# Kernel tuning notes

Measured on AMD Instinct MI355X. Metric: run time of the kernel, lower is better.

The kernel has to match this reference:

```python
import jax, jax.numpy as jnp
import numpy as np

B, N, M, D, OUT, K = 8, 32, 64, 128, 128, 3
EPS = 1e-5


def batchnorm(x, g, b):
    # training-mode BatchNorm2d over NCHW (stats over B,H,W per channel, biased var)
    mean = x.mean((0, 2, 3), keepdims=True)
    var = ((x - mean) ** 2).mean((0, 2, 3), keepdims=True)
    return g[None, :, None, None] * (x - mean) * jax.lax.rsqrt(var + EPS) + b[None, :, None, None]


def mycorr(x):
    # Pearson correlation between nodes along feature dim: x (B,M,N,D) -> (B,M,N,N)
    xc = x - x.mean(-1, keepdims=True)
    num = jnp.einsum('bmid,bmjd->bmij', xc, xc)
    nrm = jnp.sqrt((xc * xc).sum(-1))
    return num / (nrm[:, :, :, None] * nrm[:, :, None, :] + 1e-8)


def attention(x, W_fc1, W_fc2):
    # x: (B,M,N,D). AdaptiveAvgPool2d((None,1)) over the concat [Wh_i, pos*Wh_j]
    # equals 0.5*(mean_d Wh_i + mean_d(pos*Wh_j)); pos=1 where Wh_i==Wh_j else 2.
    adj = mycorr(x)
    mean_i = x.mean(-1)                       # (B,M,N)
    xi = x[:, :, :, None, :]                  # (B,M,N,1,D)
    xj = x[:, :, None, :, :]                  # (B,M,1,N,D)
    alt_mean = jnp.where(xi == xj, xj, 2.0 * xj).mean(-1)  # (B,M,N,N)
    e = 0.5 * (mean_i[:, :, :, None] + alt_mean)            # (B,M,N,N)
    ef = e.reshape(e.shape[0], e.shape[1], -1)              # (B,M,N*N) pair channels
    h = jax.nn.relu(jnp.einsum('rp,bmp->bmr', W_fc1, ef))
    e2 = jax.nn.sigmoid(jnp.einsum('pr,bmr->bmp', W_fc2, h)).reshape(e.shape)
    att = jax.nn.softmax(jnp.where(adj > 0, e2, jnp.float32(-1e12)), axis=-1)
    return jnp.einsum('bmij,bmjd->bmid', att, x)


def setup_inputs() -> dict:
    key = jax.random.key(0)
    ks = jax.random.split(key, 8)
    P, r, s = N * N, (N * N) // 2, 0.05
    return {
        'x': jax.random.normal(ks[0], (B, N, M, D), jnp.float32),
        'W_sc': jax.random.normal(ks[1], (OUT, M), jnp.float32) * s,
        'g_sc': jnp.ones(OUT, jnp.float32), 'b_sc': jnp.zeros(OUT, jnp.float32),
        'W_l1': jax.random.normal(ks[2], (M, M), jnp.float32) * s,
        'g1': jnp.ones(M, jnp.float32), 'b1': jnp.zeros(M, jnp.float32),
        'W_fc1': jax.random.normal(ks[3], (r, P), jnp.float32) * s,
        'W_fc2': jax.random.normal(ks[4], (P, r), jnp.float32) * s,
        'g2': jnp.ones(M, jnp.float32), 'b2': jnp.zeros(M, jnp.float32),
        'W_dw': jax.random.normal(ks[5], (N, 1, K, K), jnp.float32) * s,
        'g3': jnp.ones(N, jnp.float32), 'b3': jnp.zeros(N, jnp.float32),
        'W_l3': jax.random.normal(ks[6], (OUT, M), jnp.float32) * s,
    }


def reference(x, W_sc, g_sc, b_sc, W_l1, g1, b1, W_fc1, W_fc2, g2, b2, W_dw, g3, b3, W_l3):
    xm = jnp.transpose(x, (0, 2, 1, 3))  # (B,M,N,D)
    # shortcut: 1x1 conv over head channel + BN (stride=1 path)
    shortcut = batchnorm(jnp.einsum('om,bmnd->bond', W_sc, xm), g_sc, b_sc)
    # layer_1: 1x1 conv, BN, global node attention, BN, ReLU
    out = batchnorm(jnp.einsum('cm,bmnd->bcnd', W_l1, xm), g1, b1)
    out = attention(out, W_fc1, W_fc2)
    out = jax.nn.relu(batchnorm(out, g2, b2))
    # layer_2: depthwise KxK conv over (head, dim) per node, BN, ReLU
    out = jnp.transpose(out, (0, 2, 1, 3))  # (B,N,M,D)
    pad = K // 2
    out = jax.lax.conv_general_dilated(out, W_dw, (1, 1), ((pad, pad), (pad, pad)),
                                       feature_group_count=N,
                                       dimension_numbers=('NCHW', 'OIHW', 'NCHW'))
    out = jax.nn.relu(batchnorm(out, g3, b3))
    # layer_3: 1x1 conv to out_channels heads + residual
    out = jnp.transpose(out, (0, 2, 1, 3))  # (B,M,N,D)
    out = jnp.einsum('om,bmnd->bond', W_l3, out) + shortcut
    return jnp.transpose(out, (0, 2, 1, 3))  # (B,N,OUT,D)
```

## Files before the change

kernel.cpp:

```cpp
#include <hip/hip_runtime.h>
#include <math.h>

#define EPS 1e-5f


__device__ __forceinline__ void fma4(float4& a, float s, const float4& v) {
    a.x += s * v.x; a.y += s * v.y; a.z += s * v.z; a.w += s * v.w;
}

__global__ __launch_bounds__(256) void k1_w(
    const float* __restrict__ x, const float* __restrict__ Wsc,
    const float* __restrict__ Wl1, float* __restrict__ t_sc,
    float* __restrict__ t_l1, float* __restrict__ stats)
{
    int g  = blockIdx.x;
    int bn = blockIdx.y;
    int b = bn >> 5, n = bn & 31;
    __shared__ __align__(16) float s_x[64 * 128];
    __shared__ __align__(16) float s_wT[64 * 68];
    int t = threadIdx.x;

    const float4* xg = (const float4*)(x + (size_t)bn * 8192);
    for (int i = t; i < 2048; i += 256) ((float4*)s_x)[i] = xg[i];

    const float* wbase = (g < 2) ? (Wsc + (size_t)g * 64 * 64) : Wl1;
    for (int i = t; i < 1024; i += 256) {
        int m = i >> 4, rq = (i & 15) * 4;
        float4 wv;
        wv.x = wbase[(size_t)(rq + 0) * 64 + m];
        wv.y = wbase[(size_t)(rq + 1) * 64 + m];
        wv.z = wbase[(size_t)(rq + 2) * 64 + m];
        wv.w = wbase[(size_t)(rq + 3) * 64 + m];
        *(float4*)(s_wT + m * 68 + rq) = wv;
    }
    __syncthreads();

    int wv = t >> 6, lane = t & 63;
    int dl = lane & 15, g4 = lane >> 4;
    int d0 = dl * 8;
    int c0 = wv * 16 + g4 * 4;

    float4 acc[4][2];
#pragma unroll
    for (int i = 0; i < 4; i++) { acc[i][0] = make_float4(0,0,0,0); acc[i][1] = make_float4(0,0,0,0); }

    for (int m = 0; m < 64; m += 2) {
        float4 x00 = *(const float4*)(s_x + m * 128 + d0);
        float4 x01 = *(const float4*)(s_x + m * 128 + d0 + 4);
        float4 x10 = *(const float4*)(s_x + (m + 1) * 128 + d0);
        float4 x11 = *(const float4*)(s_x + (m + 1) * 128 + d0 + 4);
        float4 w0 = *(const float4*)(s_wT + m * 68 + c0);
        float4 w1 = *(const float4*)(s_wT + (m + 1) * 68 + c0);
        fma4(acc[0][0], w0.x, x00); fma4(acc[0][1], w0.x, x01);
        fma4(acc[1][0], w0.y, x00); fma4(acc[1][1], w0.y, x01);
        fma4(acc[2][0], w0.z, x00); fma4(acc[2][1], w0.z, x01);
        fma4(acc[3][0], w0.w, x00); fma4(acc[3][1], w0.w, x01);
        fma4(acc[0][0], w1.x, x10); fma4(acc[0][1], w1.x, x11);
        fma4(acc[1][0], w1.y, x10); fma4(acc[1][1], w1.y, x11);
        fma4(acc[2][0], w1.z, x10); fma4(acc[2][1], w1.z, x11);
        fma4(acc[3][0], w1.w, x10); fma4(acc[3][1], w1.w, x11);
    }

#pragma unroll
    for (int i = 0; i < 4; i++) {
        int cc = g * 64 + c0 + i;
        float4 v0 = acc[i][0], v1 = acc[i][1];
        float* dst;
        if (cc < 128) dst = t_sc + (((size_t)(b * 128 + cc)) * 32 + n) * 128 + d0;
        else          dst = t_l1 + (((size_t)(b * 64 + (cc - 128))) * 32 + n) * 128 + d0;
        *(float4*)dst = v0;
        *(float4*)(dst + 4) = v1;
        float s = v0.x + v0.y + v0.z + v0.w + v1.x + v1.y + v1.z + v1.w;
        float q = v0.x*v0.x + v0.y*v0.y + v0.z*v0.z + v0.w*v0.w
                + v1.x*v1.x + v1.y*v1.y + v1.z*v1.z + v1.w*v1.w;
#pragma unroll
        for (int off = 8; off > 0; off >>= 1) {
            s += __shfl_down(s, off, 16);
            q += __shfl_down(q, off, 16);
        }
        if (dl == 0) {
            if (cc < 128) {
                atomicAdd(&stats[cc], s);
                atomicAdd(&stats[cc + 128], q);
            } else {
                atomicAdd(&stats[256 + (cc - 128)], s);
                atomicAdd(&stats[320 + (cc - 128)], q);
            }
        }
    }
}

__global__ __launch_bounds__(256) void k2_w(
    const float* __restrict__ t_l1, const float* __restrict__ g1,
    const float* __restrict__ b1, const float* __restrict__ stats,
    float* __restrict__ y_g, float* __restrict__ E,
    unsigned int* __restrict__ maskbits)
{
    int blk = blockIdx.x;
    int bm = blk >> 1, h = blk & 1;
    int t  = threadIdx.x;
    __shared__ __align__(16) float y_s[32 * 132];
    __shared__ float S_s[32];
    __shared__ unsigned int m_s[16];
    int m = bm & 63;
    float mean = stats[256 + m] * (1.0f / 32768.0f);
    float var  = stats[320 + m] * (1.0f / 32768.0f) - mean * mean;
    float a = g1[m] * rsqrtf(var + EPS);
    float c = b1[m] - a * mean;

    if (t < 16) m_s[t] = 0u;
    const float4* src = (const float4*)(t_l1 + (size_t)bm * 4096);
    for (int i = t; i < 1024; i += 256) {
        float4 v = src[i];
        v.x = a * v.x + c; v.y = a * v.y + c; v.z = a * v.z + c; v.w = a * v.w + c;
        *(float4*)(y_s + (i >> 5) * 132 + (i & 31) * 4) = v;
    }
    __syncthreads();

    {
        int r = t >> 3, j = t & 7;
        float s = 0.f;
        const float* yr = y_s + r * 132 + j * 16;
#pragma unroll
        for (int dd = 0; dd < 16; dd++) s += yr[dd];
#pragma unroll
        for (int off = 4; off > 0; off >>= 1) s += __shfl_down(s, off, 8);
        if (j == 0) S_s[r] = s;
    }
    __syncthreads();

    int i_loc = t >> 4;
    int i = h * 16 + i_loc;
    int j0 = (t & 15) * 2;
    float dot0 = 0.f, dot1 = 0.f, eq0 = 0.f, eq1 = 0.f;
    const float* yi  = y_s + i * 132;
    const float* yj0 = y_s + j0 * 132;
    const float* yj1 = y_s + (j0 + 1) * 132;
    for (int dq = 0; dq < 32; dq++) {
        float4 a4 = *(const float4*)(yi + dq * 4);
        float4 b0 = *(const float4*)(yj0 + dq * 4);
        float4 b1v = *(const float4*)(yj1 + dq * 4);
        dot0 += a4.x * b0.x + a4.y * b0.y + a4.z * b0.z + a4.w * b0.w;
        eq0  += (a4.x == b0.x ? b0.x : 0.f) + (a4.y == b0.y ? b0.y : 0.f)
              + (a4.z == b0.z ? b0.z : 0.f) + (a4.w == b0.w ? b0.w : 0.f);
        dot1 += a4.x * b1v.x + a4.y * b1v.y + a4.z * b1v.z + a4.w * b1v.w;
        eq1  += (a4.x == b1v.x ? b1v.x : 0.f) + (a4.y == b1v.y ? b1v.y : 0.f)
              + (a4.z == b1v.z ? b1v.z : 0.f) + (a4.w == b1v.w ? b1v.w : 0.f);
    }
    float Si = S_s[i];
    float Sj0 = S_s[j0], Sj1 = S_s[j0 + 1];
    unsigned int bits = 0u;
    if (dot0 - Si * Sj0 * (1.0f / 128.0f) > 0.f) bits |= (1u << j0);
    if (dot1 - Si * Sj1 * (1.0f / 128.0f) > 0.f) bits |= (1u << (j0 + 1));
    float ev0 = (Si + 2.f * Sj0 - eq0) * (1.0f / 256.0f);
    float ev1 = (Si + 2.f * Sj1 - eq1) * (1.0f / 256.0f);
    atomicOr(&m_s[i_loc], bits);
    *(float2*)(E + (size_t)bm * 1024 + i * 32 + j0) = make_float2(ev0, ev1);
    __syncthreads();
    if (t < 16) maskbits[bm * 32 + h * 16 + t] = m_s[t];

    float4* yd = (float4*)(y_g + (size_t)bm * 4096);
    for (int idx = t; idx < 512; idx += 256) {
        int row = h * 16 + (idx >> 5), col = (idx & 31) * 4;
        yd[h * 512 + idx] = *(const float4*)(y_s + row * 132 + col);
    }
}

__global__ __launch_bounds__(256) void k3a_w(
    const float* __restrict__ A, const float* __restrict__ Bm,
    float* __restrict__ Cp)
{
    __shared__ __align__(16) float lds[4 * 2304];
    int blk = blockIdx.x;
    int kz = blk >> 8, tile = blk & 255;
    int ct = tile & 15, rt = tile >> 4;
    const float* Ab = A + kz * 512;
    const float* Bb = Bm + kz * 512;
    float* C = Cp + (size_t)kz * 262144;
    int t = threadIdx.x;
    int w = t >> 6, l = t & 63;
    int row0 = rt * 32, col0 = ct * 32;
    float* As = lds + w * 2304;
    float* Bs = As + 1152;
    int rg = l >> 3, cg = l & 7, kq = (l & 7) * 4;
    const int SLABS = 4, KROW = 1024;

    float4 acc[4];
#pragma unroll
    for (int ii = 0; ii < 4; ii++) acc[ii] = make_float4(0,0,0,0);

    float4 av[4], bv[4], av2[4], bv2[4];
    int k0 = w * 32;
#pragma unroll
    for (int rr = 0; rr < 4; rr++) {
        int r = rg + rr * 8;
        av[rr] = *(const float4*)(Ab + (size_t)(row0 + r) * KROW + k0 + kq);
        bv[rr] = *(const float4*)(Bb + (size_t)(col0 + r) * KROW + k0 + kq);
    }
    for (int s = 0; s < SLABS; s++) {
#pragma unroll
        for (int rr = 0; rr < 4; rr++) {
            int r = rg + rr * 8;
            As[(kq + 0) * 36 + r] = av[rr].x; As[(kq + 1) * 36 + r] = av[rr].y;
            As[(kq + 2) * 36 + r] = av[rr].z; As[(kq + 3) * 36 + r] = av[rr].w;
            Bs[(kq + 0) * 36 + r] = bv[rr].x; Bs[(kq + 1) * 36 + r] = bv[rr].y;
            Bs[(kq + 2) * 36 + r] = bv[rr].z; Bs[(kq + 3) * 36 + r] = bv[rr].w;
        }
        if (s + 1 < SLABS) {
            int kn = (4 * (s + 1) + w) * 32;
#pragma unroll
            for (int rr = 0; rr < 4; rr++) {
                int r = rg + rr * 8;
                av2[rr] = *(const float4*)(Ab + (size_t)(row0 + r) * KROW + kn + kq);
                bv2[rr] = *(const float4*)(Bb + (size_t)(col0 + r) * KROW + kn + kq);
            }
        }
#pragma unroll
        for (int k = 0; k < 32; k++) {
            float4 a = *(const float4*)(As + k * 36 + rg * 4);
            float4 b = *(const float4*)(Bs + k * 36 + cg * 4);
            fma4(acc[0], a.x, b); fma4(acc[1], a.y, b);
            fma4(acc[2], a.z, b); fma4(acc[3], a.w, b);
        }
#pragma unroll
        for (int rr = 0; rr < 4; rr++) { av[rr] = av2[rr]; bv[rr] = bv2[rr]; }
    }

    __syncthreads();
    float* red = lds;
#pragma unroll
    for (int ii = 0; ii < 4; ii++)
        *(float4*)(red + w * 1024 + (rg * 4 + ii) * 32 + cg * 4) = acc[ii];
    __syncthreads();

    int r = t >> 3, c4 = (t & 7) * 4;
    float4 s0 = *(const float4*)(red + r * 32 + c4);
    float4 s1 = *(const float4*)(red + 1024 + r * 32 + c4);
    float4 s2 = *(const float4*)(red + 2048 + r * 32 + c4);
    float4 s3 = *(const float4*)(red + 3072 + r * 32 + c4);
    float4 v;
    v.x = s0.x + s1.x + s2.x + s3.x;
    v.y = s0.y + s1.y + s2.y + s3.y;
    v.z = s0.z + s1.z + s2.z + s3.z;
    v.w = s0.w + s1.w + s2.w + s3.w;
    *(float4*)(C + (size_t)(row0 + r) * 512 + col0 + c4) = v;
}

__global__ __launch_bounds__(256) void k4a_w(
    const float* __restrict__ H0, const float* __restrict__ H1,
    const float* __restrict__ Bm, float* __restrict__ Cp)
{
    __shared__ __align__(16) float lds[4 * 2304];
    int blk = blockIdx.x;
    int kz = blk >> 9, tile = blk & 511;
    int ct = tile & 31, rt = tile >> 5;
    const float* H0b = H0 + kz * 256;
    const float* H1b = H1 + kz * 256;
    const float* Bb  = Bm + kz * 256;
    float* C = Cp + (size_t)kz * 524288;
    int t = threadIdx.x;
    int w = t >> 6, l = t & 63;
    int row0 = rt * 32, col0 = ct * 32;
    float* As = lds + w * 2304;
    float* Bs = As + 1152;
    int rg = l >> 3, cg = l & 7, kq = (l & 7) * 4;
    const int SLABS = 2, KROW = 512;

    float4 acc[4];
#pragma unroll
    for (int ii = 0; ii < 4; ii++) acc[ii] = make_float4(0,0,0,0);

    float4 av[4], bv[4], av2[4], bv2[4];
    int k0 = w * 32;
#pragma unroll
    for (int rr = 0; rr < 4; rr++) {
        int r = rg + rr * 8;
        size_t ai = (size_t)(row0 + r) * KROW + k0 + kq;
        float4 h0 = *(const float4*)(H0b + ai);
        float4 h1 = *(const float4*)(H1b + ai);
        av[rr].x = fmaxf(h0.x + h1.x, 0.f); av[rr].y = fmaxf(h0.y + h1.y, 0.f);
        av[rr].z = fmaxf(h0.z + h1.z, 0.f); av[rr].w = fmaxf(h0.w + h1.w, 0.f);
        bv[rr] = *(const float4*)(Bb + (size_t)(col0 + r) * KROW + k0 + kq);
    }
    for (int s = 0; s < SLABS; s++) {
#pragma unroll
        for (int rr = 0; rr < 4; rr++) {
            int r = rg + rr * 8;
            As[(kq + 0) * 36 + r] = av[rr].x; As[(kq + 1) * 36 + r] = av[rr].y;
            As[(kq + 2) * 36 + r] = av[rr].z; As[(kq + 3) * 36 + r] = av[rr].w;
            Bs[(kq + 0) * 36 + r] = bv[rr].x; Bs[(kq + 1) * 36 + r] = bv[rr].y;
            Bs[(kq + 2) * 36 + r] = bv[rr].z; Bs[(kq + 3) * 36 + r] = bv[rr].w;
        }
        if (s + 1 < SLABS) {
            int kn = (4 * (s + 1) + w) * 32;
#pragma unroll
            for (int rr = 0; rr < 4; rr++) {
                int r = rg + rr * 8;
                size_t ai = (size_t)(row0 + r) * KROW + kn + kq;
                float4 h0 = *(const float4*)(H0b + ai);
                float4 h1 = *(const float4*)(H1b + ai);
                av2[rr].x = fmaxf(h0.x + h1.x, 0.f); av2[rr].y = fmaxf(h0.y + h1.y, 0.f);
                av2[rr].z = fmaxf(h0.z + h1.z, 0.f); av2[rr].w = fmaxf(h0.w + h1.w, 0.f);
                bv2[rr] = *(const float4*)(Bb + (size_t)(col0 + r) * KROW + kn + kq);
            }
        }
#pragma unroll
        for (int k = 0; k < 32; k++) {
            float4 a = *(const float4*)(As + k * 36 + rg * 4);
            float4 b = *(const float4*)(Bs + k * 36 + cg * 4);
            fma4(acc[0], a.x, b); fma4(acc[1], a.y, b);
            fma4(acc[2], a.z, b); fma4(acc[3], a.w, b);
        }
#pragma unroll
        for (int rr = 0; rr < 4; rr++) { av[rr] = av2[rr]; bv[rr] = bv2[rr]; }
    }

    __syncthreads();
    float* red = lds;
#pragma unroll
    for (int ii = 0; ii < 4; ii++)
        *(float4*)(red + w * 1024 + (rg * 4 + ii) * 32 + cg * 4) = acc[ii];
    __syncthreads();

    int r = t >> 3, c4 = (t & 7) * 4;
    float4 s0 = *(const float4*)(red + r * 32 + c4);
    float4 s1 = *(const float4*)(red + 1024 + r * 32 + c4);
    float4 s2 = *(const float4*)(red + 2048 + r * 32 + c4);
    float4 s3 = *(const float4*)(red + 3072 + r * 32 + c4);
    float4 v;
    v.x = s0.x + s1.x + s2.x + s3.x;
    v.y = s0.y + s1.y + s2.y + s3.y;
    v.z = s0.z + s1.z + s2.z + s3.z;
    v.w = s0.w + s1.w + s2.w + s3.w;
    *(float4*)(C + (size_t)(row0 + r) * 1024 + col0 + c4) = v;
}

__global__ __launch_bounds__(256) void k5_w(
    const float* __restrict__ E2a, const float* __restrict__ E2b,
    const unsigned int* __restrict__ maskbits, const float* __restrict__ y_g,
    float* __restrict__ att_out, float* __restrict__ stats)
{
    int blk = blockIdx.x;
    int bm = blk >> 1, h = blk & 1;
    int t  = threadIdx.x;
    __shared__ __align__(16) float att_s[16 * 33];
    __shared__ __align__(16) float y_sh[32 * 128];
    __shared__ float redS[4], redQ[4];

    const float4* ysrc = (const float4*)(y_g + (size_t)bm * 4096);
    for (int i = t; i < 1024; i += 256) ((float4*)y_sh)[i] = ysrc[i];

    {
        int r_loc = t >> 4;
        int r = h * 16 + r_loc;
        int j0 = (t & 15) * 2;
        unsigned int mk = maskbits[bm * 32 + r];
        size_t eidx = (size_t)bm * 1024 + r * 32 + j0;
        float2 ea = *(const float2*)(E2a + eidx);
        float2 eb = *(const float2*)(E2b + eidx);
        float s0r = ea.x + eb.x, s1r = ea.y + eb.y;
        float e0 = 1.0f / (1.0f + expf(-s0r));
        float e1 = 1.0f / (1.0f + expf(-s1r));
        float v0 = ((mk >> (j0 + 0)) & 1u) ? e0 : -1e12f;
        float v1 = ((mk >> (j0 + 1)) & 1u) ? e1 : -1e12f;
        float mx = fmaxf(v0, v1);
#pragma unroll
        for (int off = 1; off < 16; off <<= 1) mx = fmaxf(mx, __shfl_xor(mx, off, 16));
        float x0 = __expf(v0 - mx), x1 = __expf(v1 - mx);
        float sm = x0 + x1;
#pragma unroll
        for (int off = 1; off < 16; off <<= 1) sm += __shfl_xor(sm, off, 16);
        float inv = 1.0f / sm;
        att_s[r_loc * 33 + j0 + 0] = x0 * inv;
        att_s[r_loc * 33 + j0 + 1] = x1 * inv;
    }
    __syncthreads();

    int tx = t & 31, ty = t >> 5;
    int dq = tx * 4;
    float ssum = 0.f, sq = 0.f;
#pragma unroll
    for (int ii = 0; ii < 2; ii++) {
        int i_loc = ty * 2 + ii;
        int i = h * 16 + i_loc;
        float4 acc = make_float4(0.f, 0.f, 0.f, 0.f);
        for (int j = 0; j < 32; j++) {
            float aw = att_s[i_loc * 33 + j];
            float4 yv = *(const float4*)(y_sh + j * 128 + dq);
            acc.x += aw * yv.x; acc.y += aw * yv.y;
            acc.z += aw * yv.z; acc.w += aw * yv.w;
        }
        *(float4*)(att_out + (size_t)bm * 4096 + i * 128 + dq) = acc;
        ssum += acc.x + acc.y + acc.z + acc.w;
        sq   += acc.x * acc.x + acc.y * acc.y + acc.z * acc.z + acc.w * acc.w;
    }
#pragma unroll
    for (int off = 32; off > 0; off >>= 1) {
        ssum += __shfl_down(ssum, off, 64);
        sq   += __shfl_down(sq, off, 64);
    }
    int wave = t >> 6, lane = t & 63;
    if (lane == 0) { redS[wave] = ssum; redQ[wave] = sq; }
    __syncthreads();
    if (t == 0) {
        float S = redS[0] + redS[1] + redS[2] + redS[3];
        float Q = redQ[0] + redQ[1] + redQ[2] + redQ[3];
        int m = bm & 63;
        atomicAdd(&stats[384 + m], S);
        atomicAdd(&stats[448 + m], Q);
    }
}

__global__ __launch_bounds__(256) void k6_w(
    const float* __restrict__ att_out, const float* __restrict__ Wdw,
    const float* __restrict__ g2, const float* __restrict__ b2,
    float* __restrict__ stats, float* __restrict__ v_g)
{
    int blk = blockIdx.x;
    int bn = blk >> 1, h = blk & 1;
    int b = bn >> 5, n = bn & 31;
    int dbase = h * 64;
    int t = threadIdx.x;
    __shared__ float z_s[66 * 68];
    __shared__ float a2_s[64], c2_s[64];
    __shared__ float redS[4], redQ[4];

    if (t < 64) {
        float mean = stats[384 + t] * (1.0f / 32768.0f);
        float var  = stats[448 + t] * (1.0f / 32768.0f) - mean * mean;
        float a = g2[t] * rsqrtf(var + EPS);
        a2_s[t] = a; c2_s[t] = b2[t] - a * mean;
    }
    for (int i = t; i < 66 * 68; i += 256) z_s[i] = 0.f;
    __syncthreads();

    for (int i = t; i < 1024; i += 256) {
        int m = i >> 4, c4 = (i & 15) * 4;
        float4 vv = *(const float4*)(att_out + (((size_t)(b * 64 + m)) * 32 + n) * 128 + dbase + c4);
        float a = a2_s[m], c = c2_s[m];
        float* dst = z_s + (m + 1) * 68 + 1 + c4;
        dst[0] = fmaxf(a * vv.x + c, 0.f);
        dst[1] = fmaxf(a * vv.y + c, 0.f);
        dst[2] = fmaxf(a * vv.z + c, 0.f);
        dst[3] = fmaxf(a * vv.w + c, 0.f);
    }
    if (t < 128) {
        int m = t & 63, side = t >> 6;
        int d = dbase + (side ? 64 : -1);
        if (d >= 0 && d < 128) {
            float val = att_out[(((size_t)(b * 64 + m)) * 32 + n) * 128 + d];
            z_s[(m + 1) * 68 + (side ? 65 : 0)] = fmaxf(a2_s[m] * val + c2_s[m], 0.f);
        }
    }
    float w[9];
#pragma unroll
    for (int i = 0; i < 9; i++) w[i] = Wdw[n * 9 + i];
    __syncthreads();

    int tx = t & 15, ty = t >> 4;
    int d0 = tx * 4;
    float ssum = 0.f, sq = 0.f;
#pragma unroll
    for (int rr = 0; rr < 4; rr++) {
        int hr = ty * 4 + rr;
        float o0 = 0.f, o1 = 0.f, o2 = 0.f, o3 = 0.f;
#pragma unroll
        for (int dh = 0; dh < 3; dh++) {
            const float* zr = z_s + (hr + dh) * 68 + d0;
#pragma unroll
            for (int dw = 0; dw < 3; dw++) {
                float wv = w[dh * 3 + dw];
                o0 += wv * zr[dw + 0];
                o1 += wv * zr[dw + 1];
                o2 += wv * zr[dw + 2];
                o3 += wv * zr[dw + 3];
            }
        }
        *(float4*)(v_g + ((size_t)bn * 64 + hr) * 128 + dbase + d0) = make_float4(o0, o1, o2, o3);
        ssum += o0 + o1 + o2 + o3;
        sq   += o0 * o0 + o1 * o1 + o2 * o2 + o3 * o3;
    }
#pragma unroll
    for (int off = 32; off > 0; off >>= 1) {
        ssum += __shfl_down(ssum, off, 64);
        sq   += __shfl_down(sq, off, 64);
    }
    int wave = t >> 6, lane = t & 63;
    if (lane == 0) { redS[wave] = ssum; redQ[wave] = sq; }
    __syncthreads();
    if (t == 0) {
        atomicAdd(&stats[512 + n], redS[0] + redS[1] + redS[2] + redS[3]);
        atomicAdd(&stats[544 + n], redQ[0] + redQ[1] + redQ[2] + redQ[3]);
    }
}

__global__ __launch_bounds__(256) void k7_w(
    const float* __restrict__ v_g, const float* __restrict__ t_sc,
    const float* __restrict__ Wl3, const float* __restrict__ g3,
    const float* __restrict__ b3, const float* __restrict__ gsc,
    const float* __restrict__ bsc, const float* __restrict__ stats,
    float* __restrict__ outp)
{
    int oh = blockIdx.x;
    int bn = blockIdx.y;
    int b = bn >> 5, n = bn & 31;
    int t = threadIdx.x;
    __shared__ __align__(16) float z_s[64 * 128];
    __shared__ __align__(16) float s_wT[64 * 68];

    float mean3 = stats[512 + n] * (1.0f / 65536.0f);
    float var3  = stats[544 + n] * (1.0f / 65536.0f) - mean3 * mean3;
    float a3 = g3[n] * rsqrtf(var3 + EPS);
    float c3 = b3[n] - a3 * mean3;

    const float4* vsrc = (const float4*)(v_g + (size_t)bn * 8192);
    for (int i = t; i < 2048; i += 256) {
        float4 vv = vsrc[i];
        float4 r;
        r.x = fmaxf(a3 * vv.x + c3, 0.f);
        r.y = fmaxf(a3 * vv.y + c3, 0.f);
        r.z = fmaxf(a3 * vv.z + c3, 0.f);
        r.w = fmaxf(a3 * vv.w + c3, 0.f);
        ((float4*)z_s)[i] = r;
    }
    const float* wbase = Wl3 + (size_t)oh * 64 * 64;
    for (int i = t; i < 1024; i += 256) {
        int m = i >> 4, rq = (i & 15) * 4;
        float4 wv;
        wv.x = wbase[(size_t)(rq + 0) * 64 + m];
        wv.y = wbase[(size_t)(rq + 1) * 64 + m];
        wv.z = wbase[(size_t)(rq + 2) * 64 + m];
        wv.w = wbase[(size_t)(rq + 3) * 64 + m];
        *(float4*)(s_wT + m * 68 + rq) = wv;
    }
    __syncthreads();

    int wv = t >> 6, lane = t & 63;
    int dl = lane & 15, g4 = lane >> 4;
    int d0 = dl * 8;
    int c0 = wv * 16 + g4 * 4;

    float4 acc[4][2];
#pragma unroll
    for (int i = 0; i < 4; i++) { acc[i][0] = make_float4(0,0,0,0); acc[i][1] = make_float4(0,0,0,0); }

    for (int m = 0; m < 64; m += 2) {
        float4 x00 = *(const float4*)(z_s + m * 128 + d0);
        float4 x01 = *(const float4*)(z_s + m * 128 + d0 + 4);
        float4 x10 = *(const float4*)(z_s + (m + 1) * 128 + d0);
        float4 x11 = *(const float4*)(z_s + (m + 1) * 128 + d0 + 4);
        float4 w0 = *(const float4*)(s_wT + m * 68 + c0);
        float4 w1 = *(const float4*)(s_wT + (m + 1) * 68 + c0);
        fma4(acc[0][0], w0.x, x00); fma4(acc[0][1], w0.x, x01);
        fma4(acc[1][0], w0.y, x00); fma4(acc[1][1], w0.y, x01);
        fma4(acc[2][0], w0.z, x00); fma4(acc[2][1], w0.z, x01);
        fma4(acc[3][0], w0.w, x00); fma4(acc[3][1], w0.w, x01);
        fma4(acc[0][0], w1.x, x10); fma4(acc[0][1], w1.x, x11);
        fma4(acc[1][0], w1.y, x10); fma4(acc[1][1], w1.y, x11);
        fma4(acc[2][0], w1.z, x10); fma4(acc[2][1], w1.z, x11);
        fma4(acc[3][0], w1.w, x10); fma4(acc[3][1], w1.w, x11);
    }

#pragma unroll
    for (int i = 0; i < 4; i++) {
        int o = oh * 64 + c0 + i;
        float msc = stats[o] * (1.0f / 32768.0f);
        float vsc = stats[128 + o] * (1.0f / 32768.0f) - msc * msc;
        float asc = gsc[o] * rsqrtf(vsc + EPS);
        float csc = bsc[o] - asc * msc;
        const float* ts = t_sc + (((size_t)(b * 128 + o)) * 32 + n) * 128 + d0;
        float4 t0 = *(const float4*)(ts);
        float4 t1 = *(const float4*)(ts + 4);
        float4 o0 = acc[i][0], o1 = acc[i][1];
        o0.x += asc * t0.x + csc; o0.y += asc * t0.y + csc;
        o0.z += asc * t0.z + csc; o0.w += asc * t0.w + csc;
        o1.x += asc * t1.x + csc; o1.y += asc * t1.y + csc;
        o1.z += asc * t1.z + csc; o1.w += asc * t1.w + csc;
        float* dst = outp + (((size_t)(b * 32 + n)) * 128 + o) * 128 + d0;
        *(float4*)dst = o0;
        *(float4*)(dst + 4) = o1;
    }
}

extern "C" void kernel_launch(void* const* d_in, const int* in_sizes, int n_in,
                              void* d_out, int out_size, void* d_ws, size_t ws_size,
                              hipStream_t stream)
{
    const float* x    = (const float*)d_in[0];
    const float* Wsc  = (const float*)d_in[1];
    const float* gsc  = (const float*)d_in[2];
    const float* bsc  = (const float*)d_in[3];
    const float* Wl1  = (const float*)d_in[4];
    const float* g1   = (const float*)d_in[5];
    const float* b1   = (const float*)d_in[6];
    const float* Wfc1 = (const float*)d_in[7];
    const float* Wfc2 = (const float*)d_in[8];
    const float* g2   = (const float*)d_in[9];
    const float* b2   = (const float*)d_in[10];
    const float* Wdw  = (const float*)d_in[11];
    const float* g3   = (const float*)d_in[12];
    const float* b3   = (const float*)d_in[13];
    const float* Wl3  = (const float*)d_in[14];
    float* outp = (float*)d_out;

    float* ws = (float*)d_ws;
    float* stats = ws;
    float* t_sc  = ws + 1024;
    float* t_l1  = t_sc + 4194304;
    float* y_g   = t_l1 + 2097152;
    float* E     = y_g + 2097152;
    float* H0    = E + 524288;
    float* H1    = H0 + 262144;
    float* E2a   = H1 + 262144;
    float* E2b   = E2a + 524288;
    unsigned int* maskb = (unsigned int*)(E2b + 524288);

    (void)hipMemsetAsync(stats, 0, 1024 * sizeof(float), stream);

    k1_w<<<dim3(3, 256), 256, 0, stream>>>(x, Wsc, Wl1, t_sc, t_l1, stats);
    k2_w<<<1024, 256, 0, stream>>>(t_l1, g1, b1, stats, y_g, E, maskb);
    k3a_w<<<512, 256, 0, stream>>>(E, Wfc1, H0);
    k4a_w<<<1024, 256, 0, stream>>>(H0, H1, Wfc2, E2a);
    k5_w<<<1024, 256, 0, stream>>>(E2a, E2b, maskb, y_g, t_l1, stats);
    k6_w<<<512, 256, 0, stream>>>(t_l1, Wdw, g2, b2, stats, y_g);
    k7_w<<<dim3(2, 256), 256, 0, stream>>>(y_g, t_sc, Wl3, g3, b3, gsc, bsc, stats, outp);
}
```

Baseline: 213.8 us.

## Replace fp32 FC GEMMs with bf16 MFMA kernels and fuse ReLU/sigmoid epilogues

Swaps the two split-K fp32 FMA GEMMs for the attention FC layers with bf16 MFMA 16x16x32 kernels. Weights are converted to bf16 by a new kernel on every call, and the pair-energy matrix is written as bf16. ReLU moves into the fc2 A-load, and sigmoid moves into the fc2 epilogue instead of the softmax kernel. This drops split-K partial buffers and their reductions, but lowers precision to bf16 and launches far fewer blocks (64 and 128), with no LDS staging of operands.

```diff
diff --git a/kernel.cpp b/kernel.cpp
--- a/kernel.cpp
+++ b/kernel.cpp
@@ -3,9 +3,31 @@
 
 #define EPS 1e-5f
 
+typedef __bf16 bf16x8 __attribute__((ext_vector_type(8)));
+typedef float f32x4 __attribute__((ext_vector_type(4)));
+
 
 __device__ __forceinline__ void fma4(float4& a, float s, const float4& v) {
     a.x += s * v.x; a.y += s * v.y; a.z += s * v.z; a.w += s * v.w;
+}
+
+__global__ __launch_bounds__(256) void kcvt_w(
+    const float* __restrict__ W1, const float* __restrict__ W2,
+    __bf16* __restrict__ W1b, __bf16* __restrict__ W2b)
+{
+    int id = blockIdx.x * 256 + threadIdx.x;
+    const float* src; __bf16* dst;
+    if (id < 32768) { src = W1 + (size_t)id * 16;            dst = W1b + (size_t)id * 16; }
+    else            { src = W2 + (size_t)(id - 32768) * 16;  dst = W2b + (size_t)(id - 32768) * 16; }
+#pragma unroll
+    for (int h = 0; h < 2; h++) {
+        float4 a = *(const float4*)(src + h * 8);
+        float4 b = *(const float4*)(src + h * 8 + 4);
+        bf16x8 v;
+        v[0] = (__bf16)a.x; v[1] = (__bf16)a.y; v[2] = (__bf16)a.z; v[3] = (__bf16)a.w;
+        v[4] = (__bf16)b.x; v[5] = (__bf16)b.y; v[6] = (__bf16)b.z; v[7] = (__bf16)b.w;
+        *(bf16x8*)(dst + h * 8) = v;
+    }
 }
 
 __global__ __launch_bounds__(256) void k1_w(
@@ -93,7 +115,7 @@
 __global__ __launch_bounds__(256) void k2_w(
     const float* __restrict__ t_l1, const float* __restrict__ g1,
     const float* __restrict__ b1, const float* __restrict__ stats,
-    float* __restrict__ y_g, float* __restrict__ E,
+    float* __restrict__ y_g, __bf16* __restrict__ Ebf,
     unsigned int* __restrict__ maskbits)
 {
     int blk = blockIdx.x;
@@ -155,7 +177,9 @@
     float ev0 = (Si + 2.f * Sj0 - eq0) * (1.0f / 256.0f);
     float ev1 = (Si + 2.f * Sj1 - eq1) * (1.0f / 256.0f);
     atomicOr(&m_s[i_loc], bits);
-    *(float2*)(E + (size_t)bm * 1024 + i * 32 + j0) = make_float2(ev0, ev1);
+    size_t eidx = (size_t)bm * 1024 + i * 32 + j0;
+    Ebf[eidx]     = (__bf16)ev0;
+    Ebf[eidx + 1] = (__bf16)ev1;
     __syncthreads();
     if (t < 16) maskbits[bm * 32 + h * 16 + t] = m_s[t];
 
@@ -166,179 +190,79 @@
     }
 }
 
-__global__ __launch_bounds__(256) void k3a_w(
-    const float* __restrict__ A, const float* __restrict__ Bm,
-    float* __restrict__ Cp)
-{
-    __shared__ __align__(16) float lds[4 * 2304];
-    int blk = blockIdx.x;
-    int kz = blk >> 8, tile = blk & 255;
-    int ct = tile & 15, rt = tile >> 4;
-    const float* Ab = A + kz * 512;
-    const float* Bb = Bm + kz * 512;
-    float* C = Cp + (size_t)kz * 262144;
-    int t = threadIdx.x;
-    int w = t >> 6, l = t & 63;
-    int row0 = rt * 32, col0 = ct * 32;
-    float* As = lds + w * 2304;
-    float* Bs = As + 1152;
-    int rg = l >> 3, cg = l & 7, kq = (l & 7) * 4;
-    const int SLABS = 4, KROW = 1024;
-
-    float4 acc[4];
-#pragma unroll
-    for (int ii = 0; ii < 4; ii++) acc[ii] = make_float4(0,0,0,0);
-
-    float4 av[4], bv[4], av2[4], bv2[4];
-    int k0 = w * 32;
-#pragma unroll
-    for (int rr = 0; rr < 4; rr++) {
-        int r = rg + rr * 8;
-        av[rr] = *(const float4*)(Ab + (size_t)(row0 + r) * KROW + k0 + kq);
-        bv[rr] = *(const float4*)(Bb + (size_t)(col0 + r) * KROW + k0 + kq);
-    }
-    for (int s = 0; s < SLABS; s++) {
-#pragma unroll
-        for (int rr = 0; rr < 4; rr++) {
-            int r = rg + rr * 8;
-            As[(kq + 0) * 36 + r] = av[rr].x; As[(kq + 1) * 36 + r] = av[rr].y;
-            As[(kq + 2) * 36 + r] = av[rr].z; As[(kq + 3) * 36 + r] = av[rr].w;
-            Bs[(kq + 0) * 36 + r] = bv[rr].x; Bs[(kq + 1) * 36 + r] = bv[rr].y;
-            Bs[(kq + 2) * 36 + r] = bv[rr].z; Bs[(kq + 3) * 36 + r] = bv[rr].w;
-        }
-        if (s + 1 < SLABS) {
-            int kn = (4 * (s + 1) + w) * 32;
-#pragma unroll
-            for (int rr = 0; rr < 4; rr++) {
-                int r = rg + rr * 8;
-                av2[rr] = *(const float4*)(Ab + (size_t)(row0 + r) * KROW + kn + kq);
-                bv2[rr] = *(const float4*)(Bb + (size_t)(col0 + r) * KROW + kn + kq);
-            }
-        }
-#pragma unroll
-        for (int k = 0; k < 32; k++) {
-            float4 a = *(const float4*)(As + k * 36 + rg * 4);
-            float4 b = *(const float4*)(Bs + k * 36 + cg * 4);
-            fma4(acc[0], a.x, b); fma4(acc[1], a.y, b);
-            fma4(acc[2], a.z, b); fma4(acc[3], a.w, b);
-        }
-#pragma unroll
-        for (int rr = 0; rr < 4; rr++) { av[rr] = av2[rr]; bv[rr] = bv2[rr]; }
-    }
-
-    __syncthreads();
-    float* red = lds;
-#pragma unroll
-    for (int ii = 0; ii < 4; ii++)
-        *(float4*)(red + w * 1024 + (rg * 4 + ii) * 32 + cg * 4) = acc[ii];
-    __syncthreads();
-
-    int r = t >> 3, c4 = (t & 7) * 4;
-    float4 s0 = *(const float4*)(red + r * 32 + c4);
-    float4 s1 = *(const float4*)(red + 1024 + r * 32 + c4);
-    float4 s2 = *(const float4*)(red + 2048 + r * 32 + c4);
-    float4 s3 = *(const float4*)(red + 3072 + r * 32 + c4);
-    float4 v;
-    v.x = s0.x + s1.x + s2.x + s3.x;
-    v.y = s0.y + s1.y + s2.y + s3.y;
-    v.z = s0.z + s1.z + s2.z + s3.z;
-    v.w = s0.w + s1.w + s2.w + s3.w;
-    *(float4*)(C + (size_t)(row0 + r) * 512 + col0 + c4) = v;
-}
-
-__global__ __launch_bounds__(256) void k4a_w(
-    const float* __restrict__ H0, const float* __restrict__ H1,
-    const float* __restrict__ Bm, float* __restrict__ Cp)
-{
-    __shared__ __align__(16) float lds[4 * 2304];
-    int blk = blockIdx.x;
-    int kz = blk >> 9, tile = blk & 511;
-    int ct = tile & 31, rt = tile >> 5;
-    const float* H0b = H0 + kz * 256;
-    const float* H1b = H1 + kz * 256;
-    const float* Bb  = Bm + kz * 256;
-    float* C = Cp + (size_t)kz * 524288;
-    int t = threadIdx.x;
-    int w = t >> 6, l = t & 63;
-    int row0 = rt * 32, col0 = ct * 32;
-    float* As = lds + w * 2304;
-    float* Bs = As + 1152;
-    int rg = l >> 3, cg = l & 7, kq = (l & 7) * 4;
-    const int SLABS = 2, KROW = 512;
-
-    float4 acc[4];
-#pragma unroll
-    for (int ii = 0; ii < 4; ii++) acc[ii] = make_float4(0,0,0,0);
-
-    float4 av[4], bv[4], av2[4], bv2[4];
-    int k0 = w * 32;
-#pragma unroll
-    for (int rr = 0; rr < 4; rr++) {
-        int r = rg + rr * 8;
-        size_t ai = (size_t)(row0 + r) * KROW + k0 + kq;
-        float4 h0 = *(const float4*)(H0b + ai);
-        float4 h1 = *(const float4*)(H1b + ai);
-        av[rr].x = fmaxf(h0.x + h1.x, 0.f); av[rr].y = fmaxf(h0.y + h1.y, 0.f);
-        av[rr].z = fmaxf(h0.z + h1.z, 0.f); av[rr].w = fmaxf(h0.w + h1.w, 0.f);
-        bv[rr] = *(const float4*)(Bb + (size_t)(col0 + r) * KROW + k0 + kq);
-    }
-    for (int s = 0; s < SLABS; s++) {
-#pragma unroll
-        for (int rr = 0; rr < 4; rr++) {
-            int r = rg + rr * 8;
-            As[(kq + 0) * 36 + r] = av[rr].x; As[(kq + 1) * 36 + r] = av[rr].y;
-            As[(kq + 2) * 36 + r] = av[rr].z; As[(kq + 3) * 36 + r] = av[rr].w;
-            Bs[(kq + 0) * 36 + r] = bv[rr].x; Bs[(kq + 1) * 36 + r] = bv[rr].y;
-            Bs[(kq + 2) * 36 + r] = bv[rr].z; Bs[(kq + 3) * 36 + r] = bv[rr].w;
-        }
-        if (s + 1 < SLABS) {
-            int kn = (4 * (s + 1) + w) * 32;
-#pragma unroll
-            for (int rr = 0; rr < 4; rr++) {
-                int r = rg + rr * 8;
-                size_t ai = (size_t)(row0 + r) * KROW + kn + kq;
-                float4 h0 = *(const float4*)(H0b + ai);
-                float4 h1 = *(const float4*)(H1b + ai);
-                av2[rr].x = fmaxf(h0.x + h1.x, 0.f); av2[rr].y = fmaxf(h0.y + h1.y, 0.f);
-                av2[rr].z = fmaxf(h0.z + h1.z, 0.f); av2[rr].w = fmaxf(h0.w + h1.w, 0.f);
-                bv2[rr] = *(const float4*)(Bb + (size_t)(col0 + r) * KROW + kn + kq);
-            }
-        }
-#pragma unroll
-        for (int k = 0; k < 32; k++) {
-            float4 a = *(const float4*)(As + k * 36 + rg * 4);
-            float4 b = *(const float4*)(Bs + k * 36 + cg * 4);
-            fma4(acc[0], a.x, b); fma4(acc[1], a.y, b);
-            fma4(acc[2], a.z, b); fma4(acc[3], a.w, b);
-        }
-#pragma unroll
-        for (int rr = 0; rr < 4; rr++) { av[rr] = av2[rr]; bv[rr] = bv2[rr]; }
-    }
-
-    __syncthreads();
-    float* red = lds;
-#pragma unroll
-    for (int ii = 0; ii < 4; ii++)
-        *(float4*)(red + w * 1024 + (rg * 4 + ii) * 32 + cg * 4) = acc[ii];
-    __syncthreads();
-
-    int r = t >> 3, c4 = (t & 7) * 4;
-    float4 s0 = *(const float4*)(red + r * 32 + c4);
-    float4 s1 = *(const float4*)(red + 1024 + r * 32 + c4);
-    float4 s2 = *(const float4*)(red + 2048 + r * 32 + c4);
-    float4 s3 = *(const float4*)(red + 3072 + r * 32 + c4);
-    float4 v;
-    v.x = s0.x + s1.x + s2.x + s3.x;
-    v.y = s0.y + s1.y + s2.y + s3.y;
-    v.z = s0.z + s1.z + s2.z + s3.z;
-    v.w = s0.w + s1.w + s2.w + s3.w;
-    *(float4*)(C + (size_t)(row0 + r) * 1024 + col0 + c4) = v;
+__global__ __launch_bounds__(256) void fc1_mfma(
+    const __bf16* __restrict__ Ebf, const __bf16* __restrict__ W1b,
+    float* __restrict__ H)
+{
+    int bc = blockIdx.x * 64, br = blockIdx.y * 64;
+    int t = threadIdx.x, w = t >> 6, L = t & 63;
+    int lrow = L & 15, quad = L >> 4;
+
+    const __bf16* Arow = Ebf + (size_t)(br + w * 16 + lrow) * 1024 + quad * 8;
+    const __bf16* Bbase = W1b + (size_t)quad * 8;
+
+    f32x4 acc[4] = {};
+    for (int k0 = 0; k0 < 1024; k0 += 32) {
+        bf16x8 a = *(const bf16x8*)(Arow + k0);
+#pragma unroll
+        for (int j = 0; j < 4; j++) {
+            bf16x8 b = *(const bf16x8*)(Bbase + (size_t)(bc + j * 16 + lrow) * 1024 + k0);
+            acc[j] = __builtin_amdgcn_mfma_f32_16x16x32_bf16(a, b, acc[j], 0, 0, 0);
+        }
+    }
+#pragma unroll
+    for (int j = 0; j < 4; j++) {
+        int ccol = bc + j * 16 + lrow;
+#pragma unroll
+        for (int reg = 0; reg < 4; reg++) {
+            int rrow = br + w * 16 + quad * 4 + reg;
+            H[(size_t)rrow * 512 + ccol] = acc[j][reg];
+        }
+    }
+}
+
+__global__ __launch_bounds__(256) void fc2_mfma(
+    const float* __restrict__ H, const __bf16* __restrict__ W2b,
+    float* __restrict__ E2)
+{
+    int bc = blockIdx.x * 64, br = blockIdx.y * 64;
+    int t = threadIdx.x, w = t >> 6, L = t & 63;
+    int lrow = L & 15, quad = L >> 4;
+
+    const float* Arow = H + (size_t)(br + w * 16 + lrow) * 512 + quad * 8;
+    const __bf16* Bbase = W2b + (size_t)quad * 8;
+
+    f32x4 acc[4] = {};
+    for (int k0 = 0; k0 < 512; k0 += 32) {
+        float4 h0 = *(const float4*)(Arow + k0);
+        float4 h1 = *(const float4*)(Arow + k0 + 4);
+        bf16x8 a;
+        a[0] = (__bf16)fmaxf(h0.x, 0.f); a[1] = (__bf16)fmaxf(h0.y, 0.f);
+        a[2] = (__bf16)fmaxf(h0.z, 0.f); a[3] = (__bf16)fmaxf(h0.w, 0.f);
+        a[4] = (__bf16)fmaxf(h1.x, 0.f); a[5] = (__bf16)fmaxf(h1.y, 0.f);
+        a[6] = (__bf16)fmaxf(h1.z, 0.f); a[7] = (__bf16)fmaxf(h1.w, 0.f);
+#pragma unroll
+        for (int j = 0; j < 4; j++) {
+            bf16x8 b = *(const bf16x8*)(Bbase + (size_t)(bc + j * 16 + lrow) * 512 + k0);
+            acc[j] = __builtin_amdgcn_mfma_f32_16x16x32_bf16(a, b, acc[j], 0, 0, 0);
+        }
+    }
+#pragma unroll
+    for (int j = 0; j < 4; j++) {
+        int ccol = bc + j * 16 + lrow;
+#pragma unroll
+        for (int reg = 0; reg < 4; reg++) {
+            int rrow = br + w * 16 + quad * 4 + reg;
+            float v = acc[j][reg];
+            E2[(size_t)rrow * 1024 + ccol] = 1.0f / (1.0f + expf(-v));
+        }
+    }
 }
 
 __global__ __launch_bounds__(256) void k5_w(
-    const float* __restrict__ E2a, const float* __restrict__ E2b,
-    const unsigned int* __restrict__ maskbits, const float* __restrict__ y_g,
-    float* __restrict__ att_out, float* __restrict__ stats)
+    const float* __restrict__ E2, const unsigned int* __restrict__ maskbits,
+    const float* __restrict__ y_g, float* __restrict__ att_out,
+    float* __restrict__ stats)
 {
     int blk = blockIdx.x;
     int bm = blk >> 1, h = blk & 1;
@@ -355,14 +279,9 @@
         int r = h * 16 + r_loc;
         int j0 = (t & 15) * 2;
         unsigned int mk = maskbits[bm * 32 + r];
-        size_t eidx = (size_t)bm * 1024 + r * 32 + j0;
-        float2 ea = *(const float2*)(E2a + eidx);
-        float2 eb = *(const float2*)(E2b + eidx);
-        float s0r = ea.x + eb.x, s1r = ea.y + eb.y;
-        float e0 = 1.0f / (1.0f + expf(-s0r));
-        float e1 = 1.0f / (1.0f + expf(-s1r));
-        float v0 = ((mk >> (j0 + 0)) & 1u) ? e0 : -1e12f;
-        float v1 = ((mk >> (j0 + 1)) & 1u) ? e1 : -1e12f;
+        float2 e = *(const float2*)(E2 + (size_t)bm * 1024 + r * 32 + j0);
+        float v0 = ((mk >> (j0 + 0)) & 1u) ? e.x : -1e12f;
+        float v1 = ((mk >> (j0 + 1)) & 1u) ? e.y : -1e12f;
         float mx = fmaxf(v0, v1);
 #pragma unroll
         for (int off = 1; off < 16; off <<= 1) mx = fmaxf(mx, __shfl_xor(mx, off, 16));
@@ -608,20 +527,21 @@
     float* t_sc  = ws + 1024;
     float* t_l1  = t_sc + 4194304;
     float* y_g   = t_l1 + 2097152;
-    float* E     = y_g + 2097152;
-    float* H0    = E + 524288;
-    float* H1    = H0 + 262144;
-    float* E2a   = H1 + 262144;
-    float* E2b   = E2a + 524288;
-    unsigned int* maskb = (unsigned int*)(E2b + 524288);
+    float* H     = y_g + 2097152;
+    float* E2    = H + 262144;
+    __bf16* Ebf  = (__bf16*)(E2 + 524288);
+    __bf16* W1b  = (__bf16*)(E2 + 524288 + 262144);
+    __bf16* W2b  = (__bf16*)(E2 + 524288 + 262144 + 262144);
+    unsigned int* maskb = (unsigned int*)(E2 + 524288 + 262144 + 524288);
 
     (void)hipMemsetAsync(stats, 0, 1024 * sizeof(float), stream);
 
+    kcvt_w<<<256, 256, 0, stream>>>(Wfc1, Wfc2, W1b, W2b);
     k1_w<<<dim3(3, 256), 256, 0, stream>>>(x, Wsc, Wl1, t_sc, t_l1, stats);
-    k2_w<<<1024, 256, 0, stream>>>(t_l1, g1, b1, stats, y_g, E, maskb);
-    k3a_w<<<512, 256, 0, stream>>>(E, Wfc1, H0);
-    k4a_w<<<1024, 256, 0, stream>>>(H0, H1, Wfc2, E2a);
-    k5_w<<<1024, 256, 0, stream>>>(E2a, E2b, maskb, y_g, t_l1, stats);
+    k2_w<<<1024, 256, 0, stream>>>(t_l1, g1, b1, stats, y_g, Ebf, maskb);
+    fc1_mfma<<<dim3(8, 8), 256, 0, stream>>>(Ebf, W1b, H);
+    fc2_mfma<<<dim3(16, 8), 256, 0, stream>>>(H, W2b, E2);
+    k5_w<<<1024, 256, 0, stream>>>(E2, maskb, y_g, t_l1, stats);
     k6_w<<<512, 256, 0, stream>>>(t_l1, Wdw, g2, b2, stats, y_g);
     k7_w<<<dim3(2, 256), 256, 0, stream>>>(y_g, t_sc, Wl3, g3, b3, gsc, bsc, stats, outp);
 }
```

Measured after the change: 233.0 us. 9.0% more time.
